# Kernel optimization log

Measured on AMD Instinct MI355X. Metric: run time of the kernel, lower is better.

The kernel has to match this reference:

```python
import jax, jax.numpy as jnp
import numpy as np

B, S, T, E, H = 2, 2048, 2048, 1024, 16
HD = E // H  # head_dim = 64


def setup_inputs() -> dict:
    key = jax.random.key(0)
    ks = jax.random.split(key, 12)
    sc = 1.0 / np.sqrt(E)
    inp = {
        "query": jax.random.normal(ks[0], (B, S, E), jnp.float32),
        "key": jax.random.normal(ks[1], (B, T, E), jnp.float32),
        "value": jax.random.normal(ks[2], (B, T, E), jnp.float32),
        "attn_mask": jnp.ones((S, T), jnp.int32),
        # nn.Linear params: y = x @ W.T + b
        "Wq": jax.random.normal(ks[3], (E, E), jnp.float32) * sc,
        "bq": jax.random.normal(ks[4], (E,), jnp.float32) * sc,
        "Wk": jax.random.normal(ks[5], (E, E), jnp.float32) * sc,
        "bk": jax.random.normal(ks[6], (E,), jnp.float32) * sc,
        "Wv": jax.random.normal(ks[7], (E, E), jnp.float32) * sc,
        "bv": jax.random.normal(ks[8], (E,), jnp.float32) * sc,
        "Wo": jax.random.normal(ks[9], (E, E), jnp.float32) * sc,
        "bo": jax.random.normal(ks[10], (E,), jnp.float32) * sc,
    }
    return inp


def reference(query, key, value, attn_mask, Wq, bq, Wk, bk, Wv, bv, Wo, bo):
    N, Sq, Ed = query.shape
    Tk = key.shape[1]
    # projections (torch Linear: x @ W.T + b)
    q = query @ Wq.T + bq
    k = key @ Wk.T + bk
    v = value @ Wv.T + bv
    # split heads -> (N, H, S, HD)
    q = q.reshape(N, Sq, H, HD).transpose(0, 2, 1, 3)
    k = k.reshape(N, Tk, H, HD).transpose(0, 2, 1, 3)
    v = v.reshape(N, Tk, H, HD).transpose(0, 2, 1, 3)
    # scaled dot-product scores: (N, H, S, T)
    energy = jnp.einsum("nhsd,nhtd->nhst", q, k) / jnp.sqrt(jnp.float32(HD))
    energy = jnp.where(attn_mask[None, None, :, :] == 0, -jnp.inf, energy)
    attn = jax.nn.softmax(energy, axis=3)
    # dropout is identity in eval mode
    out = jnp.einsum("nhst,nhtd->nshd", attn, v).reshape(N, Sq, Ed)
    return out @ Wo.T + bo
```

## Files before the change

### kernel.cpp

```cpp
#include <hip/hip_runtime.h>

typedef __attribute__((ext_vector_type(8))) short short8;
typedef __attribute__((ext_vector_type(4))) float f32x4;
typedef __attribute__((ext_vector_type(16))) float f32x16;

#define DEV __device__ __forceinline__

constexpr int Bb = 2, Ss = 2048, Tt = 2048, Ee = 1024, Hh = 16, HDd = 64;
constexpr int Mm = Bb * Ss;
constexpr size_t NX = (size_t)Mm * Ee;
constexpr size_t NW = (size_t)Ee * Ee;

constexpr size_t OFF_XQ   = 0;
constexpr size_t OFF_XK   = OFF_XQ + NX * 2;
constexpr size_t OFF_XV   = OFF_XK + NX * 2;
constexpr size_t OFF_WQ   = OFF_XV + NX * 2;
constexpr size_t OFF_WK   = OFF_WQ + NW * 2;
constexpr size_t OFF_WV   = OFF_WK + NW * 2;
constexpr size_t OFF_WO   = OFF_WV + NW * 2;
constexpr size_t OFF_QH   = OFF_WO + NW * 2;
constexpr size_t OFF_KH   = OFF_QH + NX * 2;
constexpr size_t OFF_VH   = OFF_KH + NX * 2;
constexpr size_t OFF_OB   = OFF_VH + NX * 2;
constexpr size_t OFF_FLAG = OFF_OB + NX * 2;

DEV unsigned short f2bf(float f) {
  union { float f; unsigned u; } v; v.f = f;
  unsigned r = v.u + 0x7fffu + ((v.u >> 16) & 1u);
  return (unsigned short)(r >> 16);
}

#define GLDS16(g, l) __builtin_amdgcn_global_load_lds(                         \
    (const __attribute__((address_space(1))) void*)(g),                        \
    (__attribute__((address_space(3))) void*)(l), 16, 0, 0)

#define PLSWAP(a, b) asm("v_permlane32_swap_b32 %0, %1" : "+v"(a), "+v"(b))
#define CVTPK(d, lo, hi_) asm("v_cvt_pk_bf16_f32 %0, %1, %2" : "=v"(d) : "v"(lo), "v"(hi_))

#if __has_builtin(__builtin_amdgcn_exp2f)
#define EXP2(x) __builtin_amdgcn_exp2f(x)
#else
#define EXP2(x) __expf((x) * 0.69314718f)
#endif

constexpr float SCLQ = 0.18033688f;

__global__ __launch_bounds__(256) void prep_kernel(
    const float* __restrict__ q, const float* __restrict__ k, const float* __restrict__ v,
    const float* __restrict__ wq, const float* __restrict__ wk,
    const float* __restrict__ wv, const float* __restrict__ wo,
    const int* __restrict__ mask,
    unsigned short* __restrict__ Xq, unsigned short* __restrict__ Xk, unsigned short* __restrict__ Xv,
    unsigned short* __restrict__ Wqb, unsigned short* __restrict__ Wkb,
    unsigned short* __restrict__ Wvb, unsigned short* __restrict__ Wob,
    int* __restrict__ flagZero)
{
  constexpr size_t NXv = NX / 4, NWv = NW / 4;
  constexpr size_t tot = 4 * NXv + 4 * NWv;
  for (size_t u = (size_t)blockIdx.x * blockDim.x + threadIdx.x; u < tot;
       u += (size_t)gridDim.x * blockDim.x) {
    if (u < 3 * NXv) {
      const float* src; unsigned short* dst; size_t off;
      if (u < NXv)            { src = q; dst = Xq; off = u; }
      else if (u < 2 * NXv)   { src = k; dst = Xk; off = u - NXv; }
      else                    { src = v; dst = Xv; off = u - 2 * NXv; }
      float4 f = ((const float4*)src)[off];
      ushort4 o; o.x = f2bf(f.x); o.y = f2bf(f.y); o.z = f2bf(f.z); o.w = f2bf(f.w);
      ((ushort4*)dst)[off] = o;
    } else if (u < 3 * NXv + 4 * NWv) {
      size_t uu = u - 3 * NXv;
      int wsel = (int)(uu / NWv); size_t off = uu % NWv;
      const float* src = wsel == 0 ? wq : wsel == 1 ? wk : wsel == 2 ? wv : wo;
      unsigned short* dst = wsel == 0 ? Wqb : wsel == 1 ? Wkb : wsel == 2 ? Wvb : Wob;
      float4 f = ((const float4*)src)[off];
      ushort4 o; o.x = f2bf(f.x); o.y = f2bf(f.y); o.z = f2bf(f.z); o.w = f2bf(f.w);
      ((ushort4*)dst)[off] = o;
    } else {
      size_t off = u - 3 * NXv - 4 * NWv;
      int4 m = ((const int4*)mask)[off];
      if (m.x == 0 || m.y == 0 || m.z == 0 || m.w == 0) *flagZero = 1;
    }
  }
}

DEV void gemm128(const unsigned short* __restrict__ A, const unsigned short* __restrict__ Bm,
                 unsigned short (*Asm)[128 * 32], unsigned short (*Bsm)[128 * 32],
                 f32x4 acc[4][4], int K)
{
  const int t = threadIdx.x;
  const int w = t >> 6, lane = t & 63;
  const int l15 = lane & 15, l4 = lane >> 4;
  const int wm = w >> 1, wn = w & 1;
  const int srow = lane >> 2;
  const int skc  = (lane & 3) * 8;
#pragma unroll
  for (int mi = 0; mi < 4; ++mi)
#pragma unroll
    for (int ni = 0; ni < 4; ++ni) acc[mi][ni] = (f32x4){0.f, 0.f, 0.f, 0.f};

#define GSTAGE(d, k0)                                                              \
  {                                                                                \
    GLDS16(A  + (size_t)(w * 16 + srow) * K + (k0) + skc,      Asm[d] + w * 512);  \
    GLDS16(A  + (size_t)(64 + w * 16 + srow) * K + (k0) + skc, Asm[d] + 2048 + w * 512); \
    GLDS16(Bm + (size_t)(w * 16 + srow) * K + (k0) + skc,      Bsm[d] + w * 512);  \
    GLDS16(Bm + (size_t)(64 + w * 16 + srow) * K + (k0) + skc, Bsm[d] + 2048 + w * 512); \
  }

  GSTAGE(0, 0)
  int it = 0;
  for (int k0 = 0; k0 < K; k0 += 32, ++it) {
    const int cur = it & 1;
    asm volatile("s_waitcnt vmcnt(0)" ::: "memory");
    __builtin_amdgcn_s_barrier();
    if (k0 + 32 < K) GSTAGE(cur ^ 1, k0 + 32)

    short8 af[4], bf[4];
#pragma unroll
    for (int mi = 0; mi < 4; ++mi)
      af[mi] = *(const short8*)&Asm[cur][(wm * 64 + mi * 16 + l15) * 32 + l4 * 8];
#pragma unroll
    for (int ni = 0; ni < 4; ++ni)
      bf[ni] = *(const short8*)&Bsm[cur][(wn * 64 + ni * 16 + l15) * 32 + l4 * 8];
    __builtin_amdgcn_s_setprio(1);
#pragma unroll
    for (int mi = 0; mi < 4; ++mi)
#pragma unroll
      for (int ni = 0; ni < 4; ++ni)
        acc[mi][ni] = __builtin_amdgcn_mfma_f32_16x16x32_bf16(af[mi], bf[ni], acc[mi][ni], 0, 0, 0);
    __builtin_amdgcn_s_setprio(0);
  }
#undef GSTAGE
}

__global__ __launch_bounds__(256, 4) void gemm_qkv(
    const unsigned short* __restrict__ Xq, const unsigned short* __restrict__ Xk,
    const unsigned short* __restrict__ Xv,
    const unsigned short* __restrict__ Wqb, const unsigned short* __restrict__ Wkb,
    const unsigned short* __restrict__ Wvb,
    const float* __restrict__ bq, const float* __restrict__ bk, const float* __restrict__ bv,
    unsigned short* __restrict__ Qh, unsigned short* __restrict__ Kh, unsigned short* __restrict__ Vh)
{
  __shared__ unsigned short Asm[2][128 * 32], Bsm[2][128 * 32];
  const int z = blockIdx.z;
  const unsigned short* A  = (z == 0) ? Xq  : (z == 1) ? Xk  : Xv;
  const unsigned short* Bw = (z == 0) ? Wqb : (z == 1) ? Wkb : Wvb;
  const float* bias        = (z == 0) ? bq  : (z == 1) ? bk  : bv;
  unsigned short* Out      = (z == 0) ? Qh  : (z == 1) ? Kh  : Vh;
  const int by = blockIdx.y, bx = blockIdx.x;
  f32x4 acc[4][4];
  gemm128(A + (size_t)by * 128 * Ee, Bw + (size_t)bx * 128 * Ee, Asm, Bsm, acc, Ee);
  const int t = threadIdx.x, w = t >> 6, lane = t & 63, l15 = lane & 15, l4 = lane >> 4;
  const int wm = w >> 1, wn = w & 1;
  if (z < 2) {
    const float osc = (z == 0) ? SCLQ : 1.0f;
#pragma unroll
    for (int ni = 0; ni < 4; ++ni) {
      int col = bx * 128 + wn * 64 + ni * 16 + l15;
      float bcol = bias[col];
      int h = col >> 6, hd = col & 63;
#pragma unroll
      for (int mi = 0; mi < 4; ++mi) {
#pragma unroll
        for (int r = 0; r < 4; ++r) {
          int row = by * 128 + wm * 64 + mi * 16 + l4 * 4 + r;
          int b = row >> 11, s = row & 2047;
          Out[(((size_t)(b * Hh + h)) * Ss + s) * HDd + hd] = f2bf((acc[mi][ni][r] + bcol) * osc);
        }
      }
    }
  } else {
#pragma unroll
    for (int ni = 0; ni < 4; ++ni) {
      int col = bx * 128 + wn * 64 + ni * 16 + l15;
      float bcol = bias[col];
      int h = col >> 6, hd = col & 63;
#pragma unroll
      for (int mi = 0; mi < 4; ++mi) {
        int row = by * 128 + wm * 64 + mi * 16 + l4 * 4;
        int b = row >> 11, s = row & 2047;
        ushort4 pk;
        pk.x = f2bf(acc[mi][ni][0] + bcol); pk.y = f2bf(acc[mi][ni][1] + bcol);
        pk.z = f2bf(acc[mi][ni][2] + bcol); pk.w = f2bf(acc[mi][ni][3] + bcol);
        *(ushort4*)&Out[((size_t)((b * Hh + h) * HDd + hd)) * Ss + s] = pk;
      }
    }
  }
}

__global__ __launch_bounds__(512) void gemm_out(
    const unsigned short* __restrict__ Ob, const unsigned short* __restrict__ Wob,
    const float* __restrict__ bo, float* __restrict__ out)
{
  __shared__ unsigned short Asm[2][128 * 32], Bsm[2][128 * 32];
  const int tid = threadIdx.x, w = tid >> 6, lane = tid & 63;
  const int l15 = lane & 15, l4 = lane >> 4;
  const int wm = w >> 1, wn = w & 1;
  const int by = blockIdx.y, bx = blockIdx.x;
  const unsigned short* A  = Ob  + (size_t)by * 128 * Ee;
  const unsigned short* Bm = Wob + (size_t)bx * 128 * Ee;
  const int grow = tid >> 2, gk = (tid & 3) * 8;
  f32x4 acc[2][4];
#pragma unroll
  for (int mi = 0; mi < 2; ++mi)
#pragma unroll
    for (int ni = 0; ni < 4; ++ni) acc[mi][ni] = (f32x4){0.f, 0.f, 0.f, 0.f};

#define GSTAGE2(d, k0)                                                   \
  {                                                                      \
    GLDS16(A  + (size_t)grow * Ee + (k0) + gk, Asm[d] + w * 512);        \
    GLDS16(Bm + (size_t)grow * Ee + (k0) + gk, Bsm[d] + w * 512);        \
  }

  GSTAGE2(0, 0)
  int it = 0;
  for (int k0 = 0; k0 < Ee; k0 += 32, ++it) {
    const int cur = it & 1;
    asm volatile("s_waitcnt vmcnt(0)" ::: "memory");
    __builtin_amdgcn_s_barrier();
    if (k0 + 32 < Ee) GSTAGE2(cur ^ 1, k0 + 32)

    short8 af[2], bf[4];
#pragma unroll
    for (int mi = 0; mi < 2; ++mi)
      af[mi] = *(const short8*)&Asm[cur][(wm * 32 + mi * 16 + l15) * 32 + l4 * 8];
#pragma unroll
    for (int ni = 0; ni < 4; ++ni)
      bf[ni] = *(const short8*)&Bsm[cur][(wn * 64 + ni * 16 + l15) * 32 + l4 * 8];
    __builtin_amdgcn_s_setprio(1);
#pragma unroll
    for (int mi = 0; mi < 2; ++mi)
#pragma unroll
      for (int ni = 0; ni < 4; ++ni)
        acc[mi][ni] = __builtin_amdgcn_mfma_f32_16x16x32_bf16(af[mi], bf[ni], acc[mi][ni], 0, 0, 0);
    __builtin_amdgcn_s_setprio(0);
  }
#undef GSTAGE2

#pragma unroll
  for (int ni = 0; ni < 4; ++ni) {
    int col = bx * 128 + wn * 64 + ni * 16 + l15;
    float bcol = bo[col];
#pragma unroll
    for (int mi = 0; mi < 2; ++mi) {
#pragma unroll
      for (int r = 0; r < 4; ++r) {
        int row = by * 128 + wm * 32 + mi * 16 + l4 * 4 + r;
        out[(size_t)row * Ee + col] = acc[mi][ni][r] + bcol;
      }
    }
  }
}

__global__ __launch_bounds__(256, 4) void attn_kernel(
    const unsigned short* __restrict__ Qh, const unsigned short* __restrict__ Kh,
    const unsigned short* __restrict__ Vh, const int* __restrict__ mask,
    const int* __restrict__ flagZero, unsigned short* __restrict__ Ob)
{
  __shared__ unsigned short Ks[2][64 * 64];
  __shared__ unsigned short Vs[2][64 * 64];
  const int bh = blockIdx.y, qt = blockIdx.x;
  const int tid = threadIdx.x, w = tid >> 6, lane = tid & 63;
  const int l31 = lane & 31, hi = lane >> 5;
  const int g = w >> 1, p = w & 1;
  const bool useMask = (*flagZero != 0);
  const size_t bhBase = (size_t)bh * Ss * HDd;
  const int s0 = qt * 64 + g * 32;

  short8 qf[4];
#pragma unroll
  for (int ks = 0; ks < 4; ++ks)
    qf[ks] = *(const short8*)&Qh[bhBase + (size_t)(s0 + l31) * 64 + ks * 16 + hi * 8];

  f32x16 o0, o1, Z16;
#pragma unroll
  for (int r = 0; r < 16; ++r) { o0[r] = 0.f; o1[r] = 0.f; Z16[r] = 0.f; }
  float l_r = 0.f;

  const int cRow = tid >> 3, cG = (tid & 7) ^ (cRow & 7);

#define STAGE(d, kt2)                                                                         \
  {                                                                                           \
    _Pragma("unroll")                                                                         \
    for (int i = 0; i < 2; ++i)                                                               \
      GLDS16(Kh + bhBase + (size_t)((kt2) + i * 32 + cRow) * 64 + cG * 8,                     \
             &Ks[d][0] + (i * 256 + w * 64) * 8);                                             \
    _Pragma("unroll")                                                                         \
    for (int i = 0; i < 2; ++i)                                                               \
      GLDS16(Vh + bhBase + (size_t)(i * 32 + cRow) * Ss + (kt2) + cG * 8,                     \
             &Vs[d][0] + (i * 256 + w * 64) * 8);                                             \
  }

  STAGE(0, 0)

  for (int t = 0; t < 32; ++t) {
    const int kt2 = t * 64, cur = t & 1;
    asm volatile("s_waitcnt vmcnt(0)" ::: "memory");
    __builtin_amdgcn_s_barrier();
    if (t + 1 < 32) STAGE(cur ^ 1, kt2 + 64)

    const unsigned short* Kc = &Ks[cur][0];
    const unsigned short* Vc = &Vs[cur][0];
    const int trow = p * 32 + l31;

    f32x16 pr;
    __builtin_amdgcn_s_setprio(1);
    {
      short8 ka = *(const short8*)&Kc[trow * 64 + ((hi ^ (l31 & 7)) * 8)];
      pr = __builtin_amdgcn_mfma_f32_32x32x16_bf16(ka, qf[0], Z16, 0, 0, 0);
#pragma unroll
      for (int ks = 1; ks < 4; ++ks) {
        short8 kb = *(const short8*)&Kc[trow * 64 + (((ks * 2 + hi) ^ (l31 & 7)) * 8)];
        pr = __builtin_amdgcn_mfma_f32_32x32x16_bf16(kb, qf[ks], pr, 0, 0, 0);
      }
    }
    __builtin_amdgcn_s_setprio(0);

    if (useMask) {
      int sg = s0 + l31;
#pragma unroll
      for (int r = 0; r < 16; ++r) {
        int tg = kt2 + p * 32 + (r & 3) + 8 * (r >> 2) + 4 * hi;
        if (mask[(size_t)sg * Tt + tg] == 0) pr[r] = -1e30f;
      }
    }

#pragma unroll
    for (int r = 0; r < 16; ++r) pr[r] = EXP2(pr[r]);
    float a0 = (pr[0] + pr[1]) + (pr[2] + pr[3]);
    float a1 = (pr[4] + pr[5]) + (pr[6] + pr[7]);
    float a2 = (pr[8] + pr[9]) + (pr[10] + pr[11]);
    float a3 = (pr[12] + pr[13]) + (pr[14] + pr[15]);
    l_r += (a0 + a1) + (a2 + a3);

    short8 pa[2];
#pragma unroll
    for (int h2 = 0; h2 < 2; ++h2) {
      unsigned c0, c1, d0, d1; const int bse = h2 * 8;
      CVTPK(c0, pr[bse + 0], pr[bse + 1]);
      CVTPK(c1, pr[bse + 2], pr[bse + 3]);
      CVTPK(d0, pr[bse + 4], pr[bse + 5]);
      CVTPK(d1, pr[bse + 6], pr[bse + 7]);
      PLSWAP(c0, d0); PLSWAP(c1, d1);
      union { unsigned u[4]; short8 s; } cc;
      cc.u[0] = c0; cc.u[1] = c1; cc.u[2] = d0; cc.u[3] = d1;
      pa[h2] = cc.s;
    }

    __builtin_amdgcn_s_setprio(1);
#pragma unroll
    for (int kb = 0; kb < 2; ++kb) {
      const int sl0 = ((p * 4 + kb * 2 + hi) ^ (l31 & 7)) * 8;
      short8 vf0 = *(const short8*)&Vc[l31 * 64 + sl0];
      short8 vf1 = *(const short8*)&Vc[(32 + l31) * 64 + sl0];
      o0 = __builtin_amdgcn_mfma_f32_32x32x16_bf16(pa[kb], vf0, o0, 0, 0, 0);
      o1 = __builtin_amdgcn_mfma_f32_32x32x16_bf16(pa[kb], vf1, o1, 0, 0, 0);
    }
    __builtin_amdgcn_s_setprio(0);
  }
#undef STAGE

  __syncthreads();

  float* Ox = (float*)&Ks[0][0];
  float* Ml = (float*)&Vs[0][0];
  float lt = l_r + __shfl_xor(l_r, 32);
  if (p == 1) {
#pragma unroll
    for (int r = 0; r < 16; ++r) {
      int sr = (r & 3) + 8 * (r >> 2) + 4 * hi;
      Ox[g * 2048 + sr * 64 + l31]      = o0[r];
      Ox[g * 2048 + sr * 64 + 32 + l31] = o1[r];
    }
    if (hi == 0) Ml[g * 32 + l31] = lt;
  }
  __syncthreads();
  if (p == 0) {
    const int b = bh >> 4, h = bh & 15;
    float ltot = lt + Ml[g * 32 + l31];
    float linv = ltot > 0.f ? 1.0f / ltot : 0.f;
#pragma unroll
    for (int r = 0; r < 16; ++r) {
      int sr = (r & 3) + 8 * (r >> 2) + 4 * hi;
      float li = __shfl(linv, sr);
      size_t rowbase = (size_t)(b * Ss + s0 + sr) * Ee + h * 64;
      Ob[rowbase + l31]      = f2bf((o0[r] + Ox[g * 2048 + sr * 64 + l31]) * li);
      Ob[rowbase + 32 + l31] = f2bf((o1[r] + Ox[g * 2048 + sr * 64 + 32 + l31]) * li);
    }
  }
}

extern "C" void kernel_launch(void* const* d_in, const int* in_sizes, int n_in,
                              void* d_out, int out_size, void* d_ws, size_t ws_size,
                              hipStream_t stream) {
  const float* q   = (const float*)d_in[0];
  const float* k   = (const float*)d_in[1];
  const float* v   = (const float*)d_in[2];
  const int*  msk  = (const int*)d_in[3];
  const float* Wq  = (const float*)d_in[4];
  const float* bq  = (const float*)d_in[5];
  const float* Wk  = (const float*)d_in[6];
  const float* bk  = (const float*)d_in[7];
  const float* Wv  = (const float*)d_in[8];
  const float* bv  = (const float*)d_in[9];
  const float* Wo  = (const float*)d_in[10];
  const float* bo  = (const float*)d_in[11];
  float* out = (float*)d_out;

  char* ws = (char*)d_ws;
  unsigned short* Xq  = (unsigned short*)(ws + OFF_XQ);
  unsigned short* Xk  = (unsigned short*)(ws + OFF_XK);
  unsigned short* Xv  = (unsigned short*)(ws + OFF_XV);
  unsigned short* Wqb = (unsigned short*)(ws + OFF_WQ);
  unsigned short* Wkb = (unsigned short*)(ws + OFF_WK);
  unsigned short* Wvb = (unsigned short*)(ws + OFF_WV);
  unsigned short* Wob = (unsigned short*)(ws + OFF_WO);
  unsigned short* Qh  = (unsigned short*)(ws + OFF_QH);
  unsigned short* Kh  = (unsigned short*)(ws + OFF_KH);
  unsigned short* Vh  = (unsigned short*)(ws + OFF_VH);
  unsigned short* Ob  = (unsigned short*)(ws + OFF_OB);
  int* flagZero       = (int*)(ws + OFF_FLAG);

  hipMemsetAsync(flagZero, 0, 4, stream);
  prep_kernel<<<4096, 256, 0, stream>>>(q, k, v, Wq, Wk, Wv, Wo, msk,
                                        Xq, Xk, Xv, Wqb, Wkb, Wvb, Wob, flagZero);
  gemm_qkv<<<dim3(8, 32, 3), 256, 0, stream>>>(Xq, Xk, Xv, Wqb, Wkb, Wvb,
                                               bq, bk, bv, Qh, Kh, Vh);
  attn_kernel<<<dim3(32, 32), 256, 0, stream>>>(Qh, Kh, Vh, msk, flagZero, Ob);
  gemm_out<<<dim3(8, 32), 512, 0, stream>>>(Ob, Wob, bo, out);
}
```

Before: 135.0 us.

## Use 8-wave GEMM tiles for QKV and split attention K/V load waits

The QKV projection GEMM now uses a shared 512-thread, 8-wave routine: each wave computes a 32x64 sub-tile instead of 64x64, and the out-projection GEMM reuses the same routine. In the attention loop, the single full vmcnt(0) wait before each tile is replaced by a partial wait on K (vmcnt(2)) and a second wait plus barrier on V before the PV MFMAs. This lets the V load overlap the QK^T and softmax work. The split wait depends on the order and count of the outstanding loads in STAGE, and it adds an extra barrier per tile.

```diff
diff --git a/kernel.cpp b/kernel.cpp
--- a/kernel.cpp
+++ b/kernel.cpp
@@ -83,56 +83,52 @@
   }
 }
 
-DEV void gemm128(const unsigned short* __restrict__ A, const unsigned short* __restrict__ Bm,
-                 unsigned short (*Asm)[128 * 32], unsigned short (*Bsm)[128 * 32],
-                 f32x4 acc[4][4], int K)
-{
-  const int t = threadIdx.x;
-  const int w = t >> 6, lane = t & 63;
+DEV void gemm128_8w(const unsigned short* __restrict__ A, const unsigned short* __restrict__ Bm,
+                    unsigned short (*Asm)[128 * 32], unsigned short (*Bsm)[128 * 32],
+                    f32x4 acc[2][4], int K)
+{
+  const int tid = threadIdx.x, w = tid >> 6, lane = tid & 63;
   const int l15 = lane & 15, l4 = lane >> 4;
   const int wm = w >> 1, wn = w & 1;
-  const int srow = lane >> 2;
-  const int skc  = (lane & 3) * 8;
-#pragma unroll
-  for (int mi = 0; mi < 4; ++mi)
+  const int grow = tid >> 2, gk = (tid & 3) * 8;
+#pragma unroll
+  for (int mi = 0; mi < 2; ++mi)
 #pragma unroll
     for (int ni = 0; ni < 4; ++ni) acc[mi][ni] = (f32x4){0.f, 0.f, 0.f, 0.f};
 
-#define GSTAGE(d, k0)                                                              \
-  {                                                                                \
-    GLDS16(A  + (size_t)(w * 16 + srow) * K + (k0) + skc,      Asm[d] + w * 512);  \
-    GLDS16(A  + (size_t)(64 + w * 16 + srow) * K + (k0) + skc, Asm[d] + 2048 + w * 512); \
-    GLDS16(Bm + (size_t)(w * 16 + srow) * K + (k0) + skc,      Bsm[d] + w * 512);  \
-    GLDS16(Bm + (size_t)(64 + w * 16 + srow) * K + (k0) + skc, Bsm[d] + 2048 + w * 512); \
-  }
-
-  GSTAGE(0, 0)
+#define GSTAGE8(d, k0)                                                   \
+  {                                                                      \
+    GLDS16(A  + (size_t)grow * K + (k0) + gk, Asm[d] + w * 512);         \
+    GLDS16(Bm + (size_t)grow * K + (k0) + gk, Bsm[d] + w * 512);         \
+  }
+
+  GSTAGE8(0, 0)
   int it = 0;
   for (int k0 = 0; k0 < K; k0 += 32, ++it) {
     const int cur = it & 1;
     asm volatile("s_waitcnt vmcnt(0)" ::: "memory");
     __builtin_amdgcn_s_barrier();
-    if (k0 + 32 < K) GSTAGE(cur ^ 1, k0 + 32)
-
-    short8 af[4], bf[4];
-#pragma unroll
-    for (int mi = 0; mi < 4; ++mi)
-      af[mi] = *(const short8*)&Asm[cur][(wm * 64 + mi * 16 + l15) * 32 + l4 * 8];
+    if (k0 + 32 < K) GSTAGE8(cur ^ 1, k0 + 32)
+
+    short8 af[2], bf[4];
+#pragma unroll
+    for (int mi = 0; mi < 2; ++mi)
+      af[mi] = *(const short8*)&Asm[cur][(wm * 32 + mi * 16 + l15) * 32 + l4 * 8];
 #pragma unroll
     for (int ni = 0; ni < 4; ++ni)
       bf[ni] = *(const short8*)&Bsm[cur][(wn * 64 + ni * 16 + l15) * 32 + l4 * 8];
     __builtin_amdgcn_s_setprio(1);
 #pragma unroll
-    for (int mi = 0; mi < 4; ++mi)
+    for (int mi = 0; mi < 2; ++mi)
 #pragma unroll
       for (int ni = 0; ni < 4; ++ni)
         acc[mi][ni] = __builtin_amdgcn_mfma_f32_16x16x32_bf16(af[mi], bf[ni], acc[mi][ni], 0, 0, 0);
     __builtin_amdgcn_s_setprio(0);
   }
-#undef GSTAGE
-}
-
-__global__ __launch_bounds__(256, 4) void gemm_qkv(
+#undef GSTAGE8
+}
+
+__global__ __launch_bounds__(512) void gemm_qkv(
     const unsigned short* __restrict__ Xq, const unsigned short* __restrict__ Xk,
     const unsigned short* __restrict__ Xv,
     const unsigned short* __restrict__ Wqb, const unsigned short* __restrict__ Wkb,
@@ -147,9 +143,10 @@
   const float* bias        = (z == 0) ? bq  : (z == 1) ? bk  : bv;
   unsigned short* Out      = (z == 0) ? Qh  : (z == 1) ? Kh  : Vh;
   const int by = blockIdx.y, bx = blockIdx.x;
-  f32x4 acc[4][4];
-  gemm128(A + (size_t)by * 128 * Ee, Bw + (size_t)bx * 128 * Ee, Asm, Bsm, acc, Ee);
-  const int t = threadIdx.x, w = t >> 6, lane = t & 63, l15 = lane & 15, l4 = lane >> 4;
+  f32x4 acc[2][4];
+  gemm128_8w(A + (size_t)by * 128 * Ee, Bw + (size_t)bx * 128 * Ee, Asm, Bsm, acc, Ee);
+  const int tid = threadIdx.x, w = tid >> 6, lane = tid & 63;
+  const int l15 = lane & 15, l4 = lane >> 4;
   const int wm = w >> 1, wn = w & 1;
   if (z < 2) {
     const float osc = (z == 0) ? SCLQ : 1.0f;
@@ -159,10 +156,10 @@
       float bcol = bias[col];
       int h = col >> 6, hd = col & 63;
 #pragma unroll
-      for (int mi = 0; mi < 4; ++mi) {
+      for (int mi = 0; mi < 2; ++mi) {
 #pragma unroll
         for (int r = 0; r < 4; ++r) {
-          int row = by * 128 + wm * 64 + mi * 16 + l4 * 4 + r;
+          int row = by * 128 + wm * 32 + mi * 16 + l4 * 4 + r;
           int b = row >> 11, s = row & 2047;
           Out[(((size_t)(b * Hh + h)) * Ss + s) * HDd + hd] = f2bf((acc[mi][ni][r] + bcol) * osc);
         }
@@ -175,8 +172,8 @@
       float bcol = bias[col];
       int h = col >> 6, hd = col & 63;
 #pragma unroll
-      for (int mi = 0; mi < 4; ++mi) {
-        int row = by * 128 + wm * 64 + mi * 16 + l4 * 4;
+      for (int mi = 0; mi < 2; ++mi) {
+        int row = by * 128 + wm * 32 + mi * 16 + l4 * 4;
         int b = row >> 11, s = row & 2047;
         ushort4 pk;
         pk.x = f2bf(acc[mi][ni][0] + bcol); pk.y = f2bf(acc[mi][ni][1] + bcol);
@@ -192,50 +189,12 @@
     const float* __restrict__ bo, float* __restrict__ out)
 {
   __shared__ unsigned short Asm[2][128 * 32], Bsm[2][128 * 32];
+  const int by = blockIdx.y, bx = blockIdx.x;
+  f32x4 acc[2][4];
+  gemm128_8w(Ob + (size_t)by * 128 * Ee, Wob + (size_t)bx * 128 * Ee, Asm, Bsm, acc, Ee);
   const int tid = threadIdx.x, w = tid >> 6, lane = tid & 63;
   const int l15 = lane & 15, l4 = lane >> 4;
   const int wm = w >> 1, wn = w & 1;
-  const int by = blockIdx.y, bx = blockIdx.x;
-  const unsigned short* A  = Ob  + (size_t)by * 128 * Ee;
-  const unsigned short* Bm = Wob + (size_t)bx * 128 * Ee;
-  const int grow = tid >> 2, gk = (tid & 3) * 8;
-  f32x4 acc[2][4];
-#pragma unroll
-  for (int mi = 0; mi < 2; ++mi)
-#pragma unroll
-    for (int ni = 0; ni < 4; ++ni) acc[mi][ni] = (f32x4){0.f, 0.f, 0.f, 0.f};
-
-#define GSTAGE2(d, k0)                                                   \
-  {                                                                      \
-    GLDS16(A  + (size_t)grow * Ee + (k0) + gk, Asm[d] + w * 512);        \
-    GLDS16(Bm + (size_t)grow * Ee + (k0) + gk, Bsm[d] + w * 512);        \
-  }
-
-  GSTAGE2(0, 0)
-  int it = 0;
-  for (int k0 = 0; k0 < Ee; k0 += 32, ++it) {
-    const int cur = it & 1;
-    asm volatile("s_waitcnt vmcnt(0)" ::: "memory");
-    __builtin_amdgcn_s_barrier();
-    if (k0 + 32 < Ee) GSTAGE2(cur ^ 1, k0 + 32)
-
-    short8 af[2], bf[4];
-#pragma unroll
-    for (int mi = 0; mi < 2; ++mi)
-      af[mi] = *(const short8*)&Asm[cur][(wm * 32 + mi * 16 + l15) * 32 + l4 * 8];
-#pragma unroll
-    for (int ni = 0; ni < 4; ++ni)
-      bf[ni] = *(const short8*)&Bsm[cur][(wn * 64 + ni * 16 + l15) * 32 + l4 * 8];
-    __builtin_amdgcn_s_setprio(1);
-#pragma unroll
-    for (int mi = 0; mi < 2; ++mi)
-#pragma unroll
-      for (int ni = 0; ni < 4; ++ni)
-        acc[mi][ni] = __builtin_amdgcn_mfma_f32_16x16x32_bf16(af[mi], bf[ni], acc[mi][ni], 0, 0, 0);
-    __builtin_amdgcn_s_setprio(0);
-  }
-#undef GSTAGE2
-
 #pragma unroll
   for (int ni = 0; ni < 4; ++ni) {
     int col = bx * 128 + wn * 64 + ni * 16 + l15;
@@ -294,7 +253,7 @@
 
   for (int t = 0; t < 32; ++t) {
     const int kt2 = t * 64, cur = t & 1;
-    asm volatile("s_waitcnt vmcnt(0)" ::: "memory");
+    asm volatile("s_waitcnt vmcnt(2)" ::: "memory");
     __builtin_amdgcn_s_barrier();
     if (t + 1 < 32) STAGE(cur ^ 1, kt2 + 64)
 
@@ -345,6 +304,10 @@
       cc.u[0] = c0; cc.u[1] = c1; cc.u[2] = d0; cc.u[3] = d1;
       pa[h2] = cc.s;
     }
+
+    if (t + 1 < 32) { asm volatile("s_waitcnt vmcnt(4)" ::: "memory"); }
+    else            { asm volatile("s_waitcnt vmcnt(0)" ::: "memory"); }
+    __builtin_amdgcn_s_barrier();
 
     __builtin_amdgcn_s_setprio(1);
 #pragma unroll
@@ -423,7 +386,7 @@
   hipMemsetAsync(flagZero, 0, 4, stream);
   prep_kernel<<<4096, 256, 0, stream>>>(q, k, v, Wq, Wk, Wv, Wo, msk,
                                         Xq, Xk, Xv, Wqb, Wkb, Wvb, Wob, flagZero);
-  gemm_qkv<<<dim3(8, 32, 3), 256, 0, stream>>>(Xq, Xk, Xv, Wqb, Wkb, Wvb,
+  gemm_qkv<<<dim3(8, 32, 3), 512, 0, stream>>>(Xq, Xk, Xv, Wqb, Wkb, Wvb,
                                                bq, bk, bv, Qh, Kh, Vh);
   attn_kernel<<<dim3(32, 32), 256, 0, stream>>>(Qh, Kh, Vh, msk, flagZero, Ob);
   gemm_out<<<dim3(8, 32), 512, 0, stream>>>(Ob, Wob, bo, out);
```

Measured after the change: 136.2 us. About the same (+0.9%).

## Software-pipeline attention loop: overlap next tile QK^T with current PV

Applied to the files above, without the earlier changes.

Restructures the attention main loop so the QK^T MFMAs for tile t+1 are interleaved with the PV MFMAs for tile t, and softmax/pack for the next tile runs after them. Loads are issued two tiles ahead with partial vmcnt waits and an extra barrier per iteration. It also moves the output GEMM main loop into a shared helper, which is a refactor. The aim is to hide exp and convert latency behind matrix work, at the cost of an extra barrier and more live registers.

```diff
diff --git a/kernel.cpp b/kernel.cpp
--- a/kernel.cpp
+++ b/kernel.cpp
@@ -132,6 +132,51 @@
 #undef GSTAGE
 }
 
+DEV void gemm128_8w(const unsigned short* __restrict__ A, const unsigned short* __restrict__ Bm,
+                    unsigned short (*Asm)[128 * 32], unsigned short (*Bsm)[128 * 32],
+                    f32x4 acc[2][4], int K)
+{
+  const int tid = threadIdx.x, w = tid >> 6, lane = tid & 63;
+  const int l15 = lane & 15, l4 = lane >> 4;
+  const int wm = w >> 1, wn = w & 1;
+  const int grow = tid >> 2, gk = (tid & 3) * 8;
+#pragma unroll
+  for (int mi = 0; mi < 2; ++mi)
+#pragma unroll
+    for (int ni = 0; ni < 4; ++ni) acc[mi][ni] = (f32x4){0.f, 0.f, 0.f, 0.f};
+
+#define GSTAGE8(d, k0)                                                   \
+  {                                                                      \
+    GLDS16(A  + (size_t)grow * K + (k0) + gk, Asm[d] + w * 512);         \
+    GLDS16(Bm + (size_t)grow * K + (k0) + gk, Bsm[d] + w * 512);         \
+  }
+
+  GSTAGE8(0, 0)
+  int it = 0;
+  for (int k0 = 0; k0 < K; k0 += 32, ++it) {
+    const int cur = it & 1;
+    asm volatile("s_waitcnt vmcnt(0)" ::: "memory");
+    __builtin_amdgcn_s_barrier();
+    if (k0 + 32 < K) GSTAGE8(cur ^ 1, k0 + 32)
+
+    short8 af[2], bf[4];
+#pragma unroll
+    for (int mi = 0; mi < 2; ++mi)
+      af[mi] = *(const short8*)&Asm[cur][(wm * 32 + mi * 16 + l15) * 32 + l4 * 8];
+#pragma unroll
+    for (int ni = 0; ni < 4; ++ni)
+      bf[ni] = *(const short8*)&Bsm[cur][(wn * 64 + ni * 16 + l15) * 32 + l4 * 8];
+    __builtin_amdgcn_s_setprio(1);
+#pragma unroll
+    for (int mi = 0; mi < 2; ++mi)
+#pragma unroll
+      for (int ni = 0; ni < 4; ++ni)
+        acc[mi][ni] = __builtin_amdgcn_mfma_f32_16x16x32_bf16(af[mi], bf[ni], acc[mi][ni], 0, 0, 0);
+    __builtin_amdgcn_s_setprio(0);
+  }
+#undef GSTAGE8
+}
+
 __global__ __launch_bounds__(256, 4) void gemm_qkv(
     const unsigned short* __restrict__ Xq, const unsigned short* __restrict__ Xk,
     const unsigned short* __restrict__ Xv,
@@ -192,50 +237,12 @@
     const float* __restrict__ bo, float* __restrict__ out)
 {
   __shared__ unsigned short Asm[2][128 * 32], Bsm[2][128 * 32];
+  const int by = blockIdx.y, bx = blockIdx.x;
+  f32x4 acc[2][4];
+  gemm128_8w(Ob + (size_t)by * 128 * Ee, Wob + (size_t)bx * 128 * Ee, Asm, Bsm, acc, Ee);
   const int tid = threadIdx.x, w = tid >> 6, lane = tid & 63;
   const int l15 = lane & 15, l4 = lane >> 4;
   const int wm = w >> 1, wn = w & 1;
-  const int by = blockIdx.y, bx = blockIdx.x;
-  const unsigned short* A  = Ob  + (size_t)by * 128 * Ee;
-  const unsigned short* Bm = Wob + (size_t)bx * 128 * Ee;
-  const int grow = tid >> 2, gk = (tid & 3) * 8;
-  f32x4 acc[2][4];
-#pragma unroll
-  for (int mi = 0; mi < 2; ++mi)
-#pragma unroll
-    for (int ni = 0; ni < 4; ++ni) acc[mi][ni] = (f32x4){0.f, 0.f, 0.f, 0.f};
-
-#define GSTAGE2(d, k0)                                                   \
-  {                                                                      \
-    GLDS16(A  + (size_t)grow * Ee + (k0) + gk, Asm[d] + w * 512);        \
-    GLDS16(Bm + (size_t)grow * Ee + (k0) + gk, Bsm[d] + w * 512);        \
-  }
-
-  GSTAGE2(0, 0)
-  int it = 0;
-  for (int k0 = 0; k0 < Ee; k0 += 32, ++it) {
-    const int cur = it & 1;
-    asm volatile("s_waitcnt vmcnt(0)" ::: "memory");
-    __builtin_amdgcn_s_barrier();
-    if (k0 + 32 < Ee) GSTAGE2(cur ^ 1, k0 + 32)
-
-    short8 af[2], bf[4];
-#pragma unroll
-    for (int mi = 0; mi < 2; ++mi)
-      af[mi] = *(const short8*)&Asm[cur][(wm * 32 + mi * 16 + l15) * 32 + l4 * 8];
-#pragma unroll
-    for (int ni = 0; ni < 4; ++ni)
-      bf[ni] = *(const short8*)&Bsm[cur][(wn * 64 + ni * 16 + l15) * 32 + l4 * 8];
-    __builtin_amdgcn_s_setprio(1);
-#pragma unroll
-    for (int mi = 0; mi < 2; ++mi)
-#pragma unroll
-      for (int ni = 0; ni < 4; ++ni)
-        acc[mi][ni] = __builtin_amdgcn_mfma_f32_16x16x32_bf16(af[mi], bf[ni], acc[mi][ni], 0, 0, 0);
-    __builtin_amdgcn_s_setprio(0);
-  }
-#undef GSTAGE2
-
 #pragma unroll
   for (int ni = 0; ni < 4; ++ni) {
     int col = bx * 128 + wn * 64 + ni * 16 + l15;
@@ -265,6 +272,7 @@
   const bool useMask = (*flagZero != 0);
   const size_t bhBase = (size_t)bh * Ss * HDd;
   const int s0 = qt * 64 + g * 32;
+  const int trow = p * 32 + l31;
 
   short8 qf[4];
 #pragma unroll
@@ -290,74 +298,103 @@
              &Vs[d][0] + (i * 256 + w * 64) * 8);                                             \
   }
 
+#define SMPACK(kt2)                                                                           \
+  {                                                                                           \
+    if (useMask) {                                                                            \
+      int sg = s0 + l31;                                                                      \
+      _Pragma("unroll")                                                                       \
+      for (int r = 0; r < 16; ++r) {                                                          \
+        int tg = (kt2) + p * 32 + (r & 3) + 8 * (r >> 2) + 4 * hi;                            \
+        if (mask[(size_t)sg * Tt + tg] == 0) pr[r] = -1e30f;                                  \
+      }                                                                                       \
+    }                                                                                         \
+    _Pragma("unroll")                                                                         \
+    for (int r = 0; r < 16; ++r) pr[r] = EXP2(pr[r]);                                         \
+    float a0 = (pr[0] + pr[1]) + (pr[2] + pr[3]);                                             \
+    float a1 = (pr[4] + pr[5]) + (pr[6] + pr[7]);                                             \
+    float a2 = (pr[8] + pr[9]) + (pr[10] + pr[11]);                                           \
+    float a3 = (pr[12] + pr[13]) + (pr[14] + pr[15]);                                         \
+    l_r += (a0 + a1) + (a2 + a3);                                                             \
+    _Pragma("unroll")                                                                         \
+    for (int h2 = 0; h2 < 2; ++h2) {                                                          \
+      unsigned c0, c1, d0, d1; const int bse = h2 * 8;                                        \
+      CVTPK(c0, pr[bse + 0], pr[bse + 1]);                                                    \
+      CVTPK(c1, pr[bse + 2], pr[bse + 3]);                                                    \
+      CVTPK(d0, pr[bse + 4], pr[bse + 5]);                                                    \
+      CVTPK(d1, pr[bse + 6], pr[bse + 7]);                                                    \
+      PLSWAP(c0, d0); PLSWAP(c1, d1);                                                         \
+      union { unsigned u[4]; short8 s; } cc;                                                  \
+      cc.u[0] = c0; cc.u[1] = c1; cc.u[2] = d0; cc.u[3] = d1;                                 \
+      pa[h2] = cc.s;                                                                          \
+    }                                                                                         \
+  }
+
+  f32x16 pr;
+  short8 pa[2];
+
   STAGE(0, 0)
+  asm volatile("s_waitcnt vmcnt(2)" ::: "memory");
+  __builtin_amdgcn_s_barrier();
+  STAGE(1, 64)
+  {
+    const unsigned short* Kc = &Ks[0][0];
+    short8 ka = *(const short8*)&Kc[trow * 64 + ((hi ^ (l31 & 7)) * 8)];
+    pr = __builtin_amdgcn_mfma_f32_32x32x16_bf16(ka, qf[0], Z16, 0, 0, 0);
+#pragma unroll
+    for (int ks = 1; ks < 4; ++ks) {
+      short8 kb = *(const short8*)&Kc[trow * 64 + (((ks * 2 + hi) ^ (l31 & 7)) * 8)];
+      pr = __builtin_amdgcn_mfma_f32_32x32x16_bf16(kb, qf[ks], pr, 0, 0, 0);
+    }
+  }
+  SMPACK(0)
 
   for (int t = 0; t < 32; ++t) {
-    const int kt2 = t * 64, cur = t & 1;
-    asm volatile("s_waitcnt vmcnt(0)" ::: "memory");
+    const int cur = t & 1;
+    if (t < 31) { asm volatile("s_waitcnt vmcnt(2)" ::: "memory"); }
+    else        { asm volatile("s_waitcnt vmcnt(0)" ::: "memory"); }
     __builtin_amdgcn_s_barrier();
-    if (t + 1 < 32) STAGE(cur ^ 1, kt2 + 64)
-
-    const unsigned short* Kc = &Ks[cur][0];
+
     const unsigned short* Vc = &Vs[cur][0];
-    const int trow = p * 32 + l31;
-
-    f32x16 pr;
     __builtin_amdgcn_s_setprio(1);
-    {
-      short8 ka = *(const short8*)&Kc[trow * 64 + ((hi ^ (l31 & 7)) * 8)];
-      pr = __builtin_amdgcn_mfma_f32_32x32x16_bf16(ka, qf[0], Z16, 0, 0, 0);
-#pragma unroll
-      for (int ks = 1; ks < 4; ++ks) {
-        short8 kb = *(const short8*)&Kc[trow * 64 + (((ks * 2 + hi) ^ (l31 & 7)) * 8)];
-        pr = __builtin_amdgcn_mfma_f32_32x32x16_bf16(kb, qf[ks], pr, 0, 0, 0);
-      }
+    if (t < 31) {
+      const unsigned short* Kn = &Ks[cur ^ 1][0];
+      short8 ka0 = *(const short8*)&Kn[trow * 64 + (((0 + hi) ^ (l31 & 7)) * 8)];
+      short8 ka1 = *(const short8*)&Kn[trow * 64 + (((2 + hi) ^ (l31 & 7)) * 8)];
+      short8 ka2 = *(const short8*)&Kn[trow * 64 + (((4 + hi) ^ (l31 & 7)) * 8)];
+      short8 ka3 = *(const short8*)&Kn[trow * 64 + (((6 + hi) ^ (l31 & 7)) * 8)];
+      short8 vf00 = *(const short8*)&Vc[l31 * 64 + (((p * 4 + 0 + hi) ^ (l31 & 7)) * 8)];
+      short8 vf01 = *(const short8*)&Vc[(32 + l31) * 64 + (((p * 4 + 0 + hi) ^ ((l31 & 7))) * 8)];
+      short8 vf10 = *(const short8*)&Vc[l31 * 64 + (((p * 4 + 2 + hi) ^ (l31 & 7)) * 8)];
+      short8 vf11 = *(const short8*)&Vc[(32 + l31) * 64 + (((p * 4 + 2 + hi) ^ ((l31 & 7))) * 8)];
+      f32x16 prN;
+      prN = __builtin_amdgcn_mfma_f32_32x32x16_bf16(ka0, qf[0], Z16, 0, 0, 0);
+      o0  = __builtin_amdgcn_mfma_f32_32x32x16_bf16(pa[0], vf00, o0, 0, 0, 0);
+      o1  = __builtin_amdgcn_mfma_f32_32x32x16_bf16(pa[0], vf01, o1, 0, 0, 0);
+      prN = __builtin_amdgcn_mfma_f32_32x32x16_bf16(ka1, qf[1], prN, 0, 0, 0);
+      o0  = __builtin_amdgcn_mfma_f32_32x32x16_bf16(pa[1], vf10, o0, 0, 0, 0);
+      prN = __builtin_amdgcn_mfma_f32_32x32x16_bf16(ka2, qf[2], prN, 0, 0, 0);
+      o1  = __builtin_amdgcn_mfma_f32_32x32x16_bf16(pa[1], vf11, o1, 0, 0, 0);
+      prN = __builtin_amdgcn_mfma_f32_32x32x16_bf16(ka3, qf[3], prN, 0, 0, 0);
+      pr = prN;
+    } else {
+      short8 vf00 = *(const short8*)&Vc[l31 * 64 + (((p * 4 + 0 + hi) ^ (l31 & 7)) * 8)];
+      short8 vf01 = *(const short8*)&Vc[(32 + l31) * 64 + (((p * 4 + 0 + hi) ^ ((l31 & 7))) * 8)];
+      short8 vf10 = *(const short8*)&Vc[l31 * 64 + (((p * 4 + 2 + hi) ^ (l31 & 7)) * 8)];
+      short8 vf11 = *(const short8*)&Vc[(32 + l31) * 64 + (((p * 4 + 2 + hi) ^ ((l31 & 7))) * 8)];
+      o0 = __builtin_amdgcn_mfma_f32_32x32x16_bf16(pa[0], vf00, o0, 0, 0, 0);
+      o1 = __builtin_amdgcn_mfma_f32_32x32x16_bf16(pa[0], vf01, o1, 0, 0, 0);
+      o0 = __builtin_amdgcn_mfma_f32_32x32x16_bf16(pa[1], vf10, o0, 0, 0, 0);
+      o1 = __builtin_amdgcn_mfma_f32_32x32x16_bf16(pa[1], vf11, o1, 0, 0, 0);
     }
     __builtin_amdgcn_s_setprio(0);
 
-    if (useMask) {
-      int sg = s0 + l31;
-#pragma unroll
-      for (int r = 0; r < 16; ++r) {
-        int tg = kt2 + p * 32 + (r & 3) + 8 * (r >> 2) + 4 * hi;
-        if (mask[(size_t)sg * Tt + tg] == 0) pr[r] = -1e30f;
-      }
-    }
-
-#pragma unroll
-    for (int r = 0; r < 16; ++r) pr[r] = EXP2(pr[r]);
-    float a0 = (pr[0] + pr[1]) + (pr[2] + pr[3]);
-    float a1 = (pr[4] + pr[5]) + (pr[6] + pr[7]);
-    float a2 = (pr[8] + pr[9]) + (pr[10] + pr[11]);
-    float a3 = (pr[12] + pr[13]) + (pr[14] + pr[15]);
-    l_r += (a0 + a1) + (a2 + a3);
-
-    short8 pa[2];
-#pragma unroll
-    for (int h2 = 0; h2 < 2; ++h2) {
-      unsigned c0, c1, d0, d1; const int bse = h2 * 8;
-      CVTPK(c0, pr[bse + 0], pr[bse + 1]);
-      CVTPK(c1, pr[bse + 2], pr[bse + 3]);
-      CVTPK(d0, pr[bse + 4], pr[bse + 5]);
-      CVTPK(d1, pr[bse + 6], pr[bse + 7]);
-      PLSWAP(c0, d0); PLSWAP(c1, d1);
-      union { unsigned u[4]; short8 s; } cc;
-      cc.u[0] = c0; cc.u[1] = c1; cc.u[2] = d0; cc.u[3] = d1;
-      pa[h2] = cc.s;
-    }
-
-    __builtin_amdgcn_s_setprio(1);
-#pragma unroll
-    for (int kb = 0; kb < 2; ++kb) {
-      const int sl0 = ((p * 4 + kb * 2 + hi) ^ (l31 & 7)) * 8;
-      short8 vf0 = *(const short8*)&Vc[l31 * 64 + sl0];
-      short8 vf1 = *(const short8*)&Vc[(32 + l31) * 64 + sl0];
-      o0 = __builtin_amdgcn_mfma_f32_32x32x16_bf16(pa[kb], vf0, o0, 0, 0, 0);
-      o1 = __builtin_amdgcn_mfma_f32_32x32x16_bf16(pa[kb], vf1, o1, 0, 0, 0);
-    }
-    __builtin_amdgcn_s_setprio(0);
+    if (t < 31) SMPACK((t + 1) * 64)
+
+    __builtin_amdgcn_s_barrier();
+    if (t < 30) STAGE(cur, (t + 2) * 64)
   }
 #undef STAGE
+#undef SMPACK
 
   __syncthreads();
 
```

New measurement: 133.0 us. About the same (-1.4%).
